# Kernel optimization log

Hardware: AMD Instinct MI355X
Metric: run time of the kernel (lower is better)

Reference implementation:

```python
import jax, jax.numpy as jnp
import numpy as np

B, N = 16, 1024
NT = 3            # atom types
NPT = 6           # pair types = NT*(NT+1)//2


def setup_inputs() -> dict:
    key = jax.random.key(0)
    ks = jax.random.split(key, 8)
    types = jax.random.randint(ks[0], (B, N), 0, NT, dtype=jnp.int32)
    n_atoms = jax.random.randint(ks[1], (B,), N // 2, N + 1, dtype=jnp.int32)
    # interatomic distances in a physically plausible range [1.5, 5.5)
    distances = 1.5 + 4.0 * jax.random.uniform(ks[2], (B, N, N), dtype=jnp.float32)
    # pair type index from (ti, tj) using combinations_with_replacement ordering
    ti = types[:, :, None]
    tj = types[:, None, :]
    lo = jnp.minimum(ti, tj)
    hi = jnp.maximum(ti, tj)
    pair_types = (lo * (2 * NT - lo + 1) // 2 + (hi - lo)).astype(jnp.int32)
    # per-pair-type potential params [a, b, r0] and density params [xi, q, r0]
    phi_params = jnp.stack([
        0.5 + jax.random.uniform(ks[3], (NPT,)),          # a
        1.0 + jax.random.uniform(ks[4], (NPT,)),          # b
        2.0 + jax.random.uniform(ks[5], (NPT,)),          # r0
    ], axis=-1).astype(jnp.float32)
    rho_params = jnp.stack([
        0.5 + jax.random.uniform(ks[6], (NPT,)),          # xi
        1.0 + jax.random.uniform(ks[7], (NPT,)),          # q
        2.0 + jax.random.uniform(jax.random.fold_in(key, 9), (NPT,)),  # r0
    ], axis=-1).astype(jnp.float32)
    emb_params = jnp.stack([
        0.5 + jax.random.uniform(jax.random.fold_in(key, 10), (NT,)),  # A (sqrt embedding)
        0.1 * jax.random.normal(jax.random.fold_in(key, 11), (NT,)),   # offset
    ], axis=-1).astype(jnp.float32)
    return {"types": types, "n_atoms": n_atoms, "distances": distances,
            "pair_types": pair_types, "phi_params": phi_params,
            "rho_params": rho_params, "emb_params": emb_params}


def reference(types, n_atoms, distances, pair_types, phi_params, rho_params, emb_params):
    # masks emulating raggedness: valid atoms and valid (i != j) pairs
    idx = jnp.arange(N)
    atom_mask = idx[None, :] < n_atoms[:, None]                      # [B, N]
    pair_mask = (atom_mask[:, :, None] & atom_mask[:, None, :]
                 & ~jnp.eye(N, dtype=bool)[None])                    # [B, N, N]

    # per-pair-type routed potential and density (branchless 'where' method)
    pp = phi_params[pair_types]                                      # [B, N, N, 3]
    phi = pp[..., 0] * jnp.exp(-pp[..., 1] * (distances - pp[..., 2]))
    rp = rho_params[pair_types]
    rho = rp[..., 0] * jnp.exp(-rp[..., 1] * (distances - rp[..., 2]))
    phi = jnp.where(pair_mask, phi, 0.0)
    rho = jnp.where(pair_mask, rho, 0.0)

    # scatter/reduce over neighbors -> per-atom quantities
    sum_rho = jnp.sum(rho * rho, axis=-1)                            # [B, N]
    sum_phi = jnp.sum(phi, axis=-1)                                  # [B, N]
    sum_rho = jnp.maximum(sum_rho, 1e-30)

    # per-atom-type embedding F(|x|) + offset
    A = emb_params[types, 0]
    off = emb_params[types, 1]
    emb = -A * jnp.sqrt(jnp.abs(sum_rho)) + off

    atomic_energies = jnp.where(atom_mask, sum_phi + emb, 0.0)       # [B, N]
    energy = jnp.sum(atomic_energies, axis=-1, keepdims=True)        # [B, 1]
    energy_per_atom = energy / n_atoms[:, None].astype(energy.dtype)
    return energy_per_atom
```

## Files before the change

kernel.cpp:

```cpp
#include <hip/hip_runtime.h>

#define NN 1024
#define BB 16
#define NTY 3

__global__ __launch_bounds__(256) void eam_rows(
    const int* __restrict__ types, const int* __restrict__ n_atoms,
    const float* __restrict__ distances,
    const float* __restrict__ phi_params, const float* __restrict__ rho_params,
    const float* __restrict__ emb_params, float* __restrict__ row_e)
{
    __shared__ int4  s_types4[NN / 4];
    __shared__ float4 s_tbl[NTY * NTY];

    const int tid = threadIdx.x;
    const int b = blockIdx.y;
    const int rowBase = blockIdx.x * 8;

    s_types4[tid] = ((const int4*)(types + b * NN))[tid];

    if (tid < NTY * NTY) {
        const int ti = tid / NTY, tj = tid % NTY;
        const int lo = min(ti, tj), hi = max(ti, tj);
        const int pt = lo * (2 * NTY - lo + 1) / 2 + (hi - lo);
        const float p0 = phi_params[pt * 3 + 0];
        const float p1 = phi_params[pt * 3 + 1];
        const float p2 = phi_params[pt * 3 + 2];
        const float r0 = rho_params[pt * 3 + 0];
        const float r1 = rho_params[pt * 3 + 1];
        const float r2 = rho_params[pt * 3 + 2];
        const float LOG2E = 1.44269504088896f;
        s_tbl[tid] = make_float4(p0 * __expf(p1 * p2), -p1 * LOG2E,
                                 r0 * __expf(r1 * r2), -r1 * LOG2E);
    }
    __syncthreads();

    const int lane = tid & 63;
    const int wave = tid >> 6;
    const int na = n_atoms[b];
    const int* s_types = (const int*)s_types4;

#pragma unroll
    for (int rr = 0; rr < 2; ++rr) {
        const int i = rowBase + wave * 2 + rr;
        if (i < na) {
            const int ti = s_types[i];
            const float4* drow =
                (const float4*)(distances + ((size_t)(b * NN + i)) * NN);
            float sph = 0.f, srh = 0.f;
#pragma unroll
            for (int pass = 0; pass < 4; ++pass) {
                const int c4 = pass * 64 + lane;
                const float4 d4 = drow[c4];
                const int4 tj4 = s_types4[c4];
                const int jb = c4 * 4;

#define EAM_EL(E, DD, TT)                                                     \
                {                                                             \
                    const float4 prm = s_tbl[ti * NTY + (TT)];                \
                    float phi = prm.x * __builtin_amdgcn_exp2f(prm.y * (DD)); \
                    float rho = prm.z * __builtin_amdgcn_exp2f(prm.w * (DD)); \
                    const int j = jb + (E);                                   \
                    if (j >= na || j == i) { phi = 0.f; rho = 0.f; }          \
                    sph += phi;                                               \
                    srh += rho * rho;                                         \
                }
                EAM_EL(0, d4.x, tj4.x)
                EAM_EL(1, d4.y, tj4.y)
                EAM_EL(2, d4.z, tj4.z)
                EAM_EL(3, d4.w, tj4.w)
#undef EAM_EL
            }
#pragma unroll
            for (int o = 32; o > 0; o >>= 1) {
                sph += __shfl_xor(sph, o, 64);
                srh += __shfl_xor(srh, o, 64);
            }
            if (lane == 0) {
                const float A   = emb_params[ti * 2 + 0];
                const float off = emb_params[ti * 2 + 1];
                row_e[b * NN + i] =
                    sph + (-A * sqrtf(fmaxf(srh, 1e-30f)) + off);
            }
        } else {
            if (lane == 0) row_e[b * NN + i] = 0.f;
        }
    }
}

__global__ __launch_bounds__(256) void eam_reduce(
    const float* __restrict__ row_e, const int* __restrict__ n_atoms,
    float* __restrict__ out)
{
    const int b = blockIdx.x;
    const int tid = threadIdx.x;
    const float4 v = ((const float4*)(row_e + b * NN))[tid];
    float s = v.x + v.y + v.z + v.w;
#pragma unroll
    for (int o = 32; o > 0; o >>= 1) s += __shfl_xor(s, o, 64);

    __shared__ float wsum[4];
    const int lane = tid & 63, wave = tid >> 6;
    if (lane == 0) wsum[wave] = s;
    __syncthreads();
    if (tid == 0) {
        const float t = wsum[0] + wsum[1] + wsum[2] + wsum[3];
        out[b] = t / (float)n_atoms[b];
    }
}

extern "C" void kernel_launch(void* const* d_in, const int* in_sizes, int n_in,
                              void* d_out, int out_size, void* d_ws, size_t ws_size,
                              hipStream_t stream) {
    const int*   types      = (const int*)d_in[0];
    const int*   n_atoms    = (const int*)d_in[1];
    const float* distances  = (const float*)d_in[2];
    const float* phi_params = (const float*)d_in[4];
    const float* rho_params = (const float*)d_in[5];
    const float* emb_params = (const float*)d_in[6];

    float* row_e = (float*)d_ws;

    eam_rows<<<dim3(NN / 8, BB), 256, 0, stream>>>(
        types, n_atoms, distances, phi_params, rho_params, emb_params, row_e);
    eam_reduce<<<BB, 256, 0, stream>>>(row_e, n_atoms, (float*)d_out);
}
```

Measured before the change: 19.79 us.

## Fold potential params into log-space quadratic, packed FMA exps, skip invalid column chunks

Each pair's prefactor and squared density are moved into the exponent, so each element costs one packed FMA plus two exp2, with no multiplies. The per-type table is replaced by a quadratic in the neighbor type evaluated with v_pk_fma_f32, which removes the shared-memory table and the barrier. Column chunks beyond n_atoms are skipped per row, and the diagonal term is subtracted afterwards instead of masked per element. The grid is remapped to one row per wave, and the reduce kernel becomes a single wave. Risks are log2 of the params (they must be positive, which holds here), and cancellation error from subtracting the self term.

```diff
diff --git a/kernel.cpp b/kernel.cpp
--- a/kernel.cpp
+++ b/kernel.cpp
@@ -3,6 +3,14 @@
 #define NN 1024
 #define BB 16
 #define NTY 3
+
+typedef float v2f __attribute__((ext_vector_type(2)));
+
+__device__ __forceinline__ v2f pk_fma(v2f a, v2f b, v2f c) {
+    v2f d;
+    asm("v_pk_fma_f32 %0, %1, %2, %3" : "=v"(d) : "v"(a), "v"(b), "v"(c));
+    return d;
+}
 
 __global__ __launch_bounds__(256) void eam_rows(
     const int* __restrict__ types, const int* __restrict__ n_atoms,
@@ -10,103 +18,130 @@
     const float* __restrict__ phi_params, const float* __restrict__ rho_params,
     const float* __restrict__ emb_params, float* __restrict__ row_e)
 {
-    __shared__ int4  s_types4[NN / 4];
-    __shared__ float4 s_tbl[NTY * NTY];
+    const int tid  = threadIdx.x;
+    const int lane = tid & 63;
+    const int wave = tid >> 6;
+    const int b    = blockIdx.x;
+    const int bx   = blockIdx.y;
+    const int i    = bx + (wave << 8);
 
-    const int tid = threadIdx.x;
-    const int b = blockIdx.y;
-    const int rowBase = blockIdx.x * 8;
+    const int na = n_atoms[b];
+    const bool valid = i < na;
+    const bool p2 = na > 512, p3 = na > 768;
 
-    s_types4[tid] = ((const int4*)(types + b * NN))[tid];
+    const int ti = types[b * NN + i];
 
-    if (tid < NTY * NTY) {
-        const int ti = tid / NTY, tj = tid % NTY;
+    const float4* drow = (const float4*)(distances + ((size_t)(b * NN + i)) * NN);
+    float4 v0 = {0,0,0,0}, v1 = {0,0,0,0}, v2 = {0,0,0,0}, v3 = {0,0,0,0};
+    float dii = 0.f;
+    if (valid) {
+        v0 = drow[lane];
+        v1 = drow[64 + lane];
+        if (p2) v2 = drow[128 + lane];
+        if (p3) v3 = drow[192 + lane];
+        dii = ((const float*)drow)[i];
+    }
+    const int4* trow = (const int4*)(types + b * NN);
+
+    const float LOG2E = 1.44269504088896f;
+    v2f PY[3], PL[3];
+#pragma unroll
+    for (int tj = 0; tj < NTY; ++tj) {
         const int lo = min(ti, tj), hi = max(ti, tj);
         const int pt = lo * (2 * NTY - lo + 1) / 2 + (hi - lo);
-        const float p0 = phi_params[pt * 3 + 0];
-        const float p1 = phi_params[pt * 3 + 1];
-        const float p2 = phi_params[pt * 3 + 2];
+        const float q0 = phi_params[pt * 3 + 0];
+        const float q1 = phi_params[pt * 3 + 1];
+        const float q2 = phi_params[pt * 3 + 2];
         const float r0 = rho_params[pt * 3 + 0];
         const float r1 = rho_params[pt * 3 + 1];
         const float r2 = rho_params[pt * 3 + 2];
-        const float LOG2E = 1.44269504088896f;
-        s_tbl[tid] = make_float4(p0 * __expf(p1 * p2), -p1 * LOG2E,
-                                 r0 * __expf(r1 * r2), -r1 * LOG2E);
+        PY[tj] = (v2f){-q1 * LOG2E, -2.0f * r1 * LOG2E};
+        PL[tj] = (v2f){__log2f(q0) + q1 * q2 * LOG2E,
+                       2.0f * (__log2f(r0) + r1 * r2 * LOG2E)};
     }
-    __syncthreads();
+    const v2f aY = 0.5f * (PY[2] - PY[1] - PY[1] + PY[0]);
+    const v2f bY = PY[1] - PY[0] - aY;
+    const v2f cY = PY[0];
+    const v2f aL = 0.5f * (PL[2] - PL[1] - PL[1] + PL[0]);
+    const v2f bL = PL[1] - PL[0] - aL;
+    const v2f cL = PL[0];
 
-    const int lane = tid & 63;
-    const int wave = tid >> 6;
-    const int na = n_atoms[b];
-    const int* s_types = (const int*)s_types4;
+    v2f acc = {0.f, 0.f};
 
+#define EAM_EL(DD, TJ, MASKED, J)                                             \
+    {                                                                         \
+        const float tf = (float)(TJ);                                         \
+        const v2f tv = {tf, tf};                                              \
+        const v2f dv = {(DD), (DD)};                                          \
+        const v2f py = pk_fma(pk_fma(aY, tv, bY), tv, cY);                    \
+        const v2f pl = pk_fma(pk_fma(aL, tv, bL), tv, cL);                    \
+        const v2f g  = pk_fma(py, dv, pl);                                    \
+        v2f e = {__builtin_amdgcn_exp2f(g.x), __builtin_amdgcn_exp2f(g.y)};   \
+        if (MASKED) { if ((J) >= na) e = (v2f){0.f, 0.f}; }                   \
+        acc += e;                                                             \
+    }
+#define EAM_PASS(P, V, MASKED)                                                \
+    {                                                                         \
+        const int c4 = (P) * 64 + lane;                                       \
+        const int4 tj4 = trow[c4];                                            \
+        const int jb = c4 * 4;                                                \
+        EAM_EL((V).x, tj4.x, MASKED, jb + 0)                                  \
+        EAM_EL((V).y, tj4.y, MASKED, jb + 1)                                  \
+        EAM_EL((V).z, tj4.z, MASKED, jb + 2)                                  \
+        EAM_EL((V).w, tj4.w, MASKED, jb + 3)                                  \
+    }
+    EAM_PASS(0, v0, false)
+    EAM_PASS(1, v1, false)
+    if (p3) {
+        EAM_PASS(2, v2, false)
+        EAM_PASS(3, v3, true)
+    } else if (p2) {
+        EAM_PASS(2, v2, true)
+    }
+#undef EAM_PASS
+#undef EAM_EL
+
+    float sph = acc.x, srh = acc.y;
 #pragma unroll
-    for (int rr = 0; rr < 2; ++rr) {
-        const int i = rowBase + wave * 2 + rr;
-        if (i < na) {
-            const int ti = s_types[i];
-            const float4* drow =
-                (const float4*)(distances + ((size_t)(b * NN + i)) * NN);
-            float sph = 0.f, srh = 0.f;
-#pragma unroll
-            for (int pass = 0; pass < 4; ++pass) {
-                const int c4 = pass * 64 + lane;
-                const float4 d4 = drow[c4];
-                const int4 tj4 = s_types4[c4];
-                const int jb = c4 * 4;
+    for (int o = 32; o > 0; o >>= 1) {
+        sph += __shfl_xor(sph, o, 64);
+        srh += __shfl_xor(srh, o, 64);
+    }
 
-#define EAM_EL(E, DD, TT)                                                     \
-                {                                                             \
-                    const float4 prm = s_tbl[ti * NTY + (TT)];                \
-                    float phi = prm.x * __builtin_amdgcn_exp2f(prm.y * (DD)); \
-                    float rho = prm.z * __builtin_amdgcn_exp2f(prm.w * (DD)); \
-                    const int j = jb + (E);                                   \
-                    if (j >= na || j == i) { phi = 0.f; rho = 0.f; }          \
-                    sph += phi;                                               \
-                    srh += rho * rho;                                         \
-                }
-                EAM_EL(0, d4.x, tj4.x)
-                EAM_EL(1, d4.y, tj4.y)
-                EAM_EL(2, d4.z, tj4.z)
-                EAM_EL(3, d4.w, tj4.w)
-#undef EAM_EL
-            }
-#pragma unroll
-            for (int o = 32; o > 0; o >>= 1) {
-                sph += __shfl_xor(sph, o, 64);
-                srh += __shfl_xor(srh, o, 64);
-            }
-            if (lane == 0) {
-                const float A   = emb_params[ti * 2 + 0];
-                const float off = emb_params[ti * 2 + 1];
-                row_e[b * NN + i] =
-                    sph + (-A * sqrtf(fmaxf(srh, 1e-30f)) + off);
-            }
-        } else {
-            if (lane == 0) row_e[b * NN + i] = 0.f;
-        }
+    float rowE = 0.f;
+    if (valid) {
+        const float tf = (float)ti;
+        const v2f tv = {tf, tf};
+        const v2f dv = {dii, dii};
+        const v2f py = pk_fma(pk_fma(aY, tv, bY), tv, cY);
+        const v2f pl = pk_fma(pk_fma(aL, tv, bL), tv, cL);
+        const v2f g  = pk_fma(py, dv, pl);
+        const float phid = __builtin_amdgcn_exp2f(g.x);
+        const float rhid = __builtin_amdgcn_exp2f(g.y);
+        const float A   = emb_params[ti * 2 + 0];
+        const float off = emb_params[ti * 2 + 1];
+        rowE = (sph - phid) +
+               (-A * sqrtf(fmaxf(srh - rhid, 1e-30f)) + off);
     }
+    if (lane == 0) row_e[b * NN + i] = rowE;
 }
 
-__global__ __launch_bounds__(256) void eam_reduce(
+__global__ __launch_bounds__(64) void eam_reduce(
     const float* __restrict__ row_e, const int* __restrict__ n_atoms,
     float* __restrict__ out)
 {
     const int b = blockIdx.x;
-    const int tid = threadIdx.x;
-    const float4 v = ((const float4*)(row_e + b * NN))[tid];
-    float s = v.x + v.y + v.z + v.w;
+    const int lane = threadIdx.x;
+    const float4* p = (const float4*)(row_e + b * NN);
+    float s = 0.f;
+#pragma unroll
+    for (int k = 0; k < 4; ++k) {
+        const float4 v = p[lane + 64 * k];
+        s += v.x + v.y + v.z + v.w;
+    }
 #pragma unroll
     for (int o = 32; o > 0; o >>= 1) s += __shfl_xor(s, o, 64);
-
-    __shared__ float wsum[4];
-    const int lane = tid & 63, wave = tid >> 6;
-    if (lane == 0) wsum[wave] = s;
-    __syncthreads();
-    if (tid == 0) {
-        const float t = wsum[0] + wsum[1] + wsum[2] + wsum[3];
-        out[b] = t / (float)n_atoms[b];
-    }
+    if (lane == 0) out[b] = s / (float)n_atoms[b];
 }
 
 extern "C" void kernel_launch(void* const* d_in, const int* in_sizes, int n_in,
@@ -121,7 +156,7 @@
 
     float* row_e = (float*)d_ws;
 
-    eam_rows<<<dim3(NN / 8, BB), 256, 0, stream>>>(
+    eam_rows<<<dim3(BB, 256), 256, 0, stream>>>(
         types, n_atoms, distances, phi_params, rho_params, emb_params, row_e);
-    eam_reduce<<<BB, 256, 0, stream>>>(row_e, n_atoms, (float*)d_out);
+    eam_reduce<<<BB, 64, 0, stream>>>(row_e, n_atoms, (float*)d_out);
 }
```

Result: slower. 21.44 us (+8.4%).
